# Kernel tuning notes

Measured on AMD Instinct MI355X. Metric: run time of the kernel, lower is better.

## Reference

```python
import jax, jax.numpy as jnp
import numpy as np


def setup_inputs() -> dict:
    key = jax.random.key(0)
    kq, kk, kv = jax.random.split(key, 3)
    B, H, S, D = 4, 16, 2048, 64
    q = jax.random.normal(kq, (B, H, S, D), dtype=jnp.float32)
    k = jax.random.normal(kk, (B, H, S, D), dtype=jnp.float32)
    v = jax.random.normal(kv, (B, H, S, D), dtype=jnp.float32)
    # causal mask: True = attend, broadcasts over batch/head dims
    mask = jnp.tril(jnp.ones((S, S), dtype=bool))
    return {"q": q, "k": k, "v": v, "mask": mask}


def reference(q, k, v, mask):
    # att[b,h,i,j] = q[b,h,i,:] . k[b,h,j,:] / sqrt(d_k)
    scale = 1.0 / jnp.sqrt(jnp.asarray(k.shape[-1], dtype=q.dtype))
    att = jnp.einsum('bhqd,bhkd->bhqk', q, k) * scale
    att = jnp.where(mask, att, -jnp.inf)  # additive -inf mask, equivalent to att + where(mask,0,-inf)
    att = jax.nn.softmax(att, axis=-1)
    return jnp.einsum('bhqk,bhkd->bhqd', att, v)
```

## Files before the change

### kernel.cpp

```cpp
#include <hip/hip_runtime.h>
#include <hip/hip_bf16.h>

typedef __attribute__((ext_vector_type(4)))  float f32x4;
typedef __attribute__((ext_vector_type(16))) float f32x16;
typedef __attribute__((ext_vector_type(8)))  short bf16x8;
typedef __attribute__((ext_vector_type(4)))  short bf16x4;

constexpr int SEQ = 2048;
constexpr int DH  = 64;
constexpr int BH  = 64;
constexpr int QB  = 256;
constexpr int KB  = 64;
constexpr int NQT = SEQ / QB;
constexpr int NST = SEQ / 64;

__device__ __forceinline__ short f2bf(float f) {
    union { float f; unsigned u; } x; x.f = f;
    unsigned r = x.u + 0x7fffu + ((x.u >> 16) & 1u);
    return (short)(r >> 16);
}

__device__ __forceinline__ unsigned cvtpk(float lo, float hi) {
    unsigned r;
    asm("v_cvt_pk_bf16_f32 %0, %1, %2" : "=v"(r) : "v"(lo), "v"(hi));
    return r;
}

__device__ __forceinline__ float exp2fast(float x) {
#if __has_builtin(__builtin_amdgcn_exp2f)
    return __builtin_amdgcn_exp2f(x);
#else
    float r;
    asm("v_exp_f32 %0, %1\n\ts_nop 0" : "=v"(r) : "v"(x));
    return r;
#endif
}

__device__ __forceinline__ void half_swap(unsigned a, unsigned b, unsigned &x, unsigned &y) {
#if __has_builtin(__builtin_amdgcn_permlane32_swap)
    auto rr = __builtin_amdgcn_permlane32_swap(a, b, false, false);
    x = rr[0]; y = rr[1];
#else
    unsigned as = (unsigned)__shfl_xor((int)a, 32);
    unsigned bs = (unsigned)__shfl_xor((int)b, 32);
    const bool lo = ((threadIdx.x & 63) < 32);
    x = lo ? a : bs;
    y = lo ? as : b;
#endif
}

__global__ __launch_bounds__(256) void prep_kernel(
    const float* __restrict__ Kg, const float* __restrict__ Vg,
    short* __restrict__ Kb, short* __restrict__ Vt)
{
    __shared__ short sT[64][66];
    const int bid = blockIdx.x;
    const int bh  = bid & (BH - 1);
    const int st  = bid >> 6;
    const int s0  = st * 64;
    const size_t base = (size_t)bh * SEQ * DH;
    const int tid = threadIdx.x;

    #pragma unroll
    for (int it = 0; it < 4; ++it) {
        const int i4 = it * 256 + tid;
        const int r  = i4 >> 4;
        const int c4 = (i4 & 15) << 2;
        const size_t gidx = base + (size_t)(s0 + r) * DH + c4;
        f32x4 kx = *(const f32x4*)(Kg + gidx);
        bf16x4 kb4;
        #pragma unroll
        for (int j = 0; j < 4; ++j) kb4[j] = f2bf(kx[j]);
        *(bf16x4*)(Kb + gidx) = kb4;
        f32x4 vx = *(const f32x4*)(Vg + gidx);
        #pragma unroll
        for (int j = 0; j < 4; ++j) sT[r][c4 + j] = f2bf(vx[j]);
    }
    __syncthreads();

    const int d   = tid >> 2;
    const int seg = (tid & 3) * 16;
    bf16x8 lo, hi;
    #pragma unroll
    for (int m = 0; m < 8; ++m) { lo[m] = sT[seg + m][d]; hi[m] = sT[seg + 8 + m][d]; }
    short* Vo = Vt + base + (size_t)d * SEQ + (s0 + seg);
    *(bf16x8*)Vo       = lo;
    *(bf16x8*)(Vo + 8) = hi;
}

__global__ __launch_bounds__(512) void fattn2_kernel(
    const float* __restrict__ Qg, const short* __restrict__ Kb,
    const short* __restrict__ Vt, float* __restrict__ Og)
{
    __shared__ short sK[KB * DH];
    __shared__ short sV[DH * KB];

    const int bid = blockIdx.x;
    const int g   = bid >> 6;
    const int bh  = bid & 63;
    const int qt  = (g < 4) ? (7 - g) : (g - 4);
    const int q0  = qt * QB;

    const int tid  = threadIdx.x;
    const int wid  = tid >> 6;
    const int lane = tid & 63;
    const int l31  = lane & 31;
    const int hi   = lane >> 5;

    const size_t base = (size_t)bh * SEQ * DH;
    const float* Qb = Qg + base;
    const short* Kp = Kb + base;
    const short* Vp = Vt + base;

    const int qw = q0 + wid * 32;
    const int qr = qw + l31;

    constexpr float QSCALE = 0.125f * 1.44269504088896340736f;
    bf16x8 qf[4];
    #pragma unroll
    for (int dt = 0; dt < 4; ++dt) {
        const float* qp = Qb + (size_t)qr * DH + dt * 16 + hi * 8;
        f32x4 a = *(const f32x4*)qp;
        f32x4 b = *(const f32x4*)(qp + 4);
        bf16x8 f;
        #pragma unroll
        for (int j = 0; j < 4; ++j) { f[j] = f2bf(a[j] * QSCALE); f[j + 4] = f2bf(b[j] * QSCALE); }
        qf[dt] = f;
    }

    f32x16 o0, o1;
    #pragma unroll
    for (int r = 0; r < 16; ++r) { o0[r] = 0.f; o1[r] = 0.f; }
    float m_i = -1e30f, l_i = 0.f;

    const int ntile = qt * 4 + 4;
    for (int t = 0; t < ntile; ++t) {
        const int kv0 = t * KB;
        __syncthreads();
        {
            const int r  = tid >> 3;
            const int cb = (tid & 7) * 16;
            bf16x8 kx = *(const bf16x8*)((const char*)(Kp + (size_t)(kv0 + r) * DH) + cb);
            *(bf16x8*)((char*)sK + r * 128 + (cb ^ ((r & 7) << 4))) = kx;
            bf16x8 vx = *(const bf16x8*)((const char*)(Vp + (size_t)r * SEQ + kv0) + cb);
            *(bf16x8*)((char*)sV + r * 128 + (cb ^ ((r & 7) << 4))) = vx;
        }
        __syncthreads();

        if (kv0 > qw + 31) continue;

        f32x16 st0, st1;
        #pragma unroll
        for (int r = 0; r < 16; ++r) { st0[r] = 0.f; st1[r] = 0.f; }
        #pragma unroll
        for (int dt = 0; dt < 4; ++dt) {
            const int ca = dt * 32 + hi * 16;
            bf16x8 k0 = *(const bf16x8*)((const char*)sK + l31 * 128 + (ca ^ ((l31 & 7) << 4)));
            bf16x8 k1 = *(const bf16x8*)((const char*)sK + (32 + l31) * 128 + (ca ^ ((l31 & 7) << 4)));
            st0 = __builtin_amdgcn_mfma_f32_32x32x16_bf16(k0, qf[dt], st0, 0, 0, 0);
            st1 = __builtin_amdgcn_mfma_f32_32x32x16_bf16(k1, qf[dt], st1, 0, 0, 0);
        }

        if (kv0 + KB - 1 > qw) {
            #pragma unroll
            for (int r = 0; r < 16; ++r) {
                const int kr = (r & 3) + 8 * (r >> 2) + 4 * hi;
                if (kv0 + kr > qr)      st0[r] = -1e30f;
                if (kv0 + 32 + kr > qr) st1[r] = -1e30f;
            }
        }

        float pm = st0[0];
        #pragma unroll
        for (int r = 1; r < 16; ++r) pm = fmaxf(pm, st0[r]);
        #pragma unroll
        for (int r = 0; r < 16; ++r) pm = fmaxf(pm, st1[r]);
        pm = fmaxf(pm, __shfl_xor(pm, 32));

        constexpr float THR = 8.0f * 1.44269504088896340736f;
        if (!__all(pm - m_i <= THR)) {
            const float nm = fmaxf(m_i, pm);
            const float cf = exp2fast(m_i - nm);
            #pragma unroll
            for (int r = 0; r < 16; ++r) {
                const int kr = (r & 3) + 8 * (r >> 2) + 4 * hi;
                const float cfr = __shfl(cf, kr);
                o0[r] *= cfr; o1[r] *= cfr;
            }
            l_i *= cf;
            m_i = nm;
        }

        float rs = 0.f;
        #pragma unroll
        for (int r = 0; r < 16; ++r) { st0[r] = exp2fast(st0[r] - m_i); rs += st0[r]; }
        #pragma unroll
        for (int r = 0; r < 16; ++r) { st1[r] = exp2fast(st1[r] - m_i); rs += st1[r]; }
        rs += __shfl_xor(rs, 32);
        l_i += rs;

        bf16x8 pf[4];
        {
            unsigned pk[8];
            #pragma unroll
            for (int i = 0; i < 8; ++i) pk[i] = cvtpk(st0[2 * i], st0[2 * i + 1]);
            #pragma unroll
            for (int c = 0; c < 2; ++c) {
                unsigned x0, y0, x1, y1;
                half_swap(pk[4 * c + 0], pk[4 * c + 2], x0, y0);
                half_swap(pk[4 * c + 1], pk[4 * c + 3], x1, y1);
                union { unsigned u[4]; bf16x8 v; } uu;
                uu.u[0] = x0; uu.u[1] = x1; uu.u[2] = y0; uu.u[3] = y1;
                pf[c] = uu.v;
            }
            #pragma unroll
            for (int i = 0; i < 8; ++i) pk[i] = cvtpk(st1[2 * i], st1[2 * i + 1]);
            #pragma unroll
            for (int c = 0; c < 2; ++c) {
                unsigned x0, y0, x1, y1;
                half_swap(pk[4 * c + 0], pk[4 * c + 2], x0, y0);
                half_swap(pk[4 * c + 1], pk[4 * c + 3], x1, y1);
                union { unsigned u[4]; bf16x8 v; } uu;
                uu.u[0] = x0; uu.u[1] = x1; uu.u[2] = y0; uu.u[3] = y1;
                pf[2 + c] = uu.v;
            }
        }

        #pragma unroll
        for (int ks = 0; ks < 4; ++ks) {
            const int cv = ks * 32 + hi * 16;
            bf16x8 v0 = *(const bf16x8*)((const char*)sV + l31 * 128 + (cv ^ ((l31 & 7) << 4)));
            o0 = __builtin_amdgcn_mfma_f32_32x32x16_bf16(pf[ks], v0, o0, 0, 0, 0);
            bf16x8 v1 = *(const bf16x8*)((const char*)sV + (32 + l31) * 128 + (cv ^ ((l31 & 7) << 4)));
            o1 = __builtin_amdgcn_mfma_f32_32x32x16_bf16(pf[ks], v1, o1, 0, 0, 0);
        }
    }

    float* Ob = Og + base;
    #pragma unroll
    for (int r = 0; r < 16; ++r) {
        const int kr  = (r & 3) + 8 * (r >> 2) + 4 * hi;
        const float ll = __shfl(l_i, kr);
        const float inv = 1.0f / ll;
        const int row = qw + kr;
        Ob[(size_t)row * DH + l31]      = o0[r] * inv;
        Ob[(size_t)row * DH + 32 + l31] = o1[r] * inv;
    }
}

extern "C" void kernel_launch(void* const* d_in, const int* in_sizes, int n_in,
                              void* d_out, int out_size, void* d_ws, size_t ws_size,
                              hipStream_t stream) {
    const float* q = (const float*)d_in[0];
    const float* k = (const float*)d_in[1];
    const float* v = (const float*)d_in[2];
    float* out = (float*)d_out;

    short* Kb = (short*)d_ws;
    short* Vt = Kb + (size_t)BH * SEQ * DH;

    prep_kernel<<<dim3(BH * NST), dim3(256), 0, stream>>>(k, v, Kb, Vt);
    fattn2_kernel<<<dim3(BH * NQT), dim3(512), 0, stream>>>(q, Kb, Vt, out);
}
```

Before: 81.48 us.

## Halve query tile, prefetch next K/V tile into registers during compute

The query block shrinks from 256 to 128 rows with 256-thread blocks and a min-blocks-per-SM launch bound of 4, doubling the grid to raise occupancy and improve causal load balance. Block scheduling becomes a simple heaviest-first order. Each iteration now issues global loads for the next K/V tile into registers before computing the current tile, then writes them to shared memory after a barrier, so memory latency overlaps the MFMA work. In exchange there is more register pressure, K/V tiles are re-read by twice as many blocks, and there are still two barriers per tile.

```diff
diff --git a/kernel.cpp b/kernel.cpp
--- a/kernel.cpp
+++ b/kernel.cpp
@@ -9,7 +9,7 @@
 constexpr int SEQ = 2048;
 constexpr int DH  = 64;
 constexpr int BH  = 64;
-constexpr int QB  = 256;
+constexpr int QB  = 128;
 constexpr int KB  = 64;
 constexpr int NQT = SEQ / QB;
 constexpr int NST = SEQ / 64;
@@ -88,7 +88,7 @@
     *(bf16x8*)(Vo + 8) = hi;
 }
 
-__global__ __launch_bounds__(512) void fattn2_kernel(
+__global__ __launch_bounds__(256, 4) void fattn3_kernel(
     const float* __restrict__ Qg, const short* __restrict__ Kb,
     const short* __restrict__ Vt, float* __restrict__ Og)
 {
@@ -96,9 +96,8 @@
     __shared__ short sV[DH * KB];
 
     const int bid = blockIdx.x;
-    const int g   = bid >> 6;
     const int bh  = bid & 63;
-    const int qt  = (g < 4) ? (7 - g) : (g - 4);
+    const int qt  = NQT - 1 - (bid >> 6);
     const int q0  = qt * QB;
 
     const int tid  = threadIdx.x;
@@ -114,6 +113,26 @@
 
     const int qw = q0 + wid * 32;
     const int qr = qw + l31;
+
+    const int r0 = tid >> 3;
+    const int c0 = tid & 7;
+    const int r1 = 32 + r0;
+    const int c1 = c0;
+
+    bf16x8 kreg0, kreg1, vreg0, vreg1;
+    auto LOAD = [&](int t) {
+        const int kv0 = t * KB;
+        kreg0 = *(const bf16x8*)(Kp + (size_t)(kv0 + r0) * DH + c0 * 8);
+        kreg1 = *(const bf16x8*)(Kp + (size_t)(kv0 + r1) * DH + c1 * 8);
+        vreg0 = *(const bf16x8*)(Vp + (size_t)r0 * SEQ + kv0 + c0 * 8);
+        vreg1 = *(const bf16x8*)(Vp + (size_t)r1 * SEQ + kv0 + c1 * 8);
+    };
+    auto WRITE = [&]() {
+        *(bf16x8*)((char*)sK + r0 * 128 + ((c0 * 16) ^ ((r0 & 7) << 4))) = kreg0;
+        *(bf16x8*)((char*)sK + r1 * 128 + ((c1 * 16) ^ ((r1 & 7) << 4))) = kreg1;
+        *(bf16x8*)((char*)sV + r0 * 128 + ((c0 * 16) ^ ((r0 & 7) << 4))) = vreg0;
+        *(bf16x8*)((char*)sV + r1 * 128 + ((c1 * 16) ^ ((r1 & 7) << 4))) = vreg1;
+    };
 
     constexpr float QSCALE = 0.125f * 1.44269504088896340736f;
     bf16x8 qf[4];
@@ -133,107 +152,106 @@
     for (int r = 0; r < 16; ++r) { o0[r] = 0.f; o1[r] = 0.f; }
     float m_i = -1e30f, l_i = 0.f;
 
-    const int ntile = qt * 4 + 4;
+    const int ntile = 2 * qt + 2;
+    LOAD(0);
+    WRITE();
+    __syncthreads();
+
     for (int t = 0; t < ntile; ++t) {
         const int kv0 = t * KB;
+        if (t + 1 < ntile) LOAD(t + 1);
+
+        if (kv0 <= qw + 31) {
+            f32x16 st0, st1;
+            #pragma unroll
+            for (int r = 0; r < 16; ++r) { st0[r] = 0.f; st1[r] = 0.f; }
+            #pragma unroll
+            for (int dt = 0; dt < 4; ++dt) {
+                const int ca = dt * 32 + hi * 16;
+                bf16x8 k0 = *(const bf16x8*)((const char*)sK + l31 * 128 + (ca ^ ((l31 & 7) << 4)));
+                bf16x8 k1 = *(const bf16x8*)((const char*)sK + (32 + l31) * 128 + (ca ^ ((l31 & 7) << 4)));
+                st0 = __builtin_amdgcn_mfma_f32_32x32x16_bf16(k0, qf[dt], st0, 0, 0, 0);
+                st1 = __builtin_amdgcn_mfma_f32_32x32x16_bf16(k1, qf[dt], st1, 0, 0, 0);
+            }
+
+            if (kv0 + KB - 1 > qw) {
+                #pragma unroll
+                for (int r = 0; r < 16; ++r) {
+                    const int kr = (r & 3) + 8 * (r >> 2) + 4 * hi;
+                    if (kv0 + kr > qr)      st0[r] = -1e30f;
+                    if (kv0 + 32 + kr > qr) st1[r] = -1e30f;
+                }
+            }
+
+            float pm = st0[0];
+            #pragma unroll
+            for (int r = 1; r < 16; ++r) pm = fmaxf(pm, st0[r]);
+            #pragma unroll
+            for (int r = 0; r < 16; ++r) pm = fmaxf(pm, st1[r]);
+            pm = fmaxf(pm, __shfl_xor(pm, 32));
+
+            constexpr float THR = 8.0f * 1.44269504088896340736f;
+            if (!__all(pm - m_i <= THR)) {
+                const float nm = fmaxf(m_i, pm);
+                const float cf = exp2fast(m_i - nm);
+                #pragma unroll
+                for (int r = 0; r < 16; ++r) {
+                    const int kr = (r & 3) + 8 * (r >> 2) + 4 * hi;
+                    const float cfr = __shfl(cf, kr);
+                    o0[r] *= cfr; o1[r] *= cfr;
+                }
+                l_i *= cf;
+                m_i = nm;
+            }
+
+            float rs = 0.f;
+            #pragma unroll
+            for (int r = 0; r < 16; ++r) { st0[r] = exp2fast(st0[r] - m_i); rs += st0[r]; }
+            #pragma unroll
+            for (int r = 0; r < 16; ++r) { st1[r] = exp2fast(st1[r] - m_i); rs += st1[r]; }
+            rs += __shfl_xor(rs, 32);
+            l_i += rs;
+
+            bf16x8 pf[4];
+            {
+                unsigned pk[8];
+                #pragma unroll
+                for (int i = 0; i < 8; ++i) pk[i] = cvtpk(st0[2 * i], st0[2 * i + 1]);
+                #pragma unroll
+                for (int c = 0; c < 2; ++c) {
+                    unsigned x0, y0, x1, y1;
+                    half_swap(pk[4 * c + 0], pk[4 * c + 2], x0, y0);
+                    half_swap(pk[4 * c + 1], pk[4 * c + 3], x1, y1);
+                    union { unsigned u[4]; bf16x8 v; } uu;
+                    uu.u[0] = x0; uu.u[1] = x1; uu.u[2] = y0; uu.u[3] = y1;
+                    pf[c] = uu.v;
+                }
+                #pragma unroll
+                for (int i = 0; i < 8; ++i) pk[i] = cvtpk(st1[2 * i], st1[2 * i + 1]);
+                #pragma unroll
+                for (int c = 0; c < 2; ++c) {
+                    unsigned x0, y0, x1, y1;
+                    half_swap(pk[4 * c + 0], pk[4 * c + 2], x0, y0);
+                    half_swap(pk[4 * c + 1], pk[4 * c + 3], x1, y1);
+                    union { unsigned u[4]; bf16x8 v; } uu;
+                    uu.u[0] = x0; uu.u[1] = x1; uu.u[2] = y0; uu.u[3] = y1;
+                    pf[2 + c] = uu.v;
+                }
+            }
+
+            #pragma unroll
+            for (int ks = 0; ks < 4; ++ks) {
+                const int cv = ks * 32 + hi * 16;
+                bf16x8 v0 = *(const bf16x8*)((const char*)sV + l31 * 128 + (cv ^ ((l31 & 7) << 4)));
+                o0 = __builtin_amdgcn_mfma_f32_32x32x16_bf16(pf[ks], v0, o0, 0, 0, 0);
+                bf16x8 v1 = *(const bf16x8*)((const char*)sV + (32 + l31) * 128 + (cv ^ ((l31 & 7) << 4)));
+                o1 = __builtin_amdgcn_mfma_f32_32x32x16_bf16(pf[ks], v1, o1, 0, 0, 0);
+            }
+        }
+
         __syncthreads();
-        {
-            const int r  = tid >> 3;
-            const int cb = (tid & 7) * 16;
-            bf16x8 kx = *(const bf16x8*)((const char*)(Kp + (size_t)(kv0 + r) * DH) + cb);
-            *(bf16x8*)((char*)sK + r * 128 + (cb ^ ((r & 7) << 4))) = kx;
-            bf16x8 vx = *(const bf16x8*)((const char*)(Vp + (size_t)r * SEQ + kv0) + cb);
-            *(bf16x8*)((char*)sV + r * 128 + (cb ^ ((r & 7) << 4))) = vx;
-        }
+        if (t + 1 < ntile) WRITE();
         __syncthreads();
-
-        if (kv0 > qw + 31) continue;
-
-        f32x16 st0, st1;
-        #pragma unroll
-        for (int r = 0; r < 16; ++r) { st0[r] = 0.f; st1[r] = 0.f; }
-        #pragma unroll
-        for (int dt = 0; dt < 4; ++dt) {
-            const int ca = dt * 32 + hi * 16;
-            bf16x8 k0 = *(const bf16x8*)((const char*)sK + l31 * 128 + (ca ^ ((l31 & 7) << 4)));
-            bf16x8 k1 = *(const bf16x8*)((const char*)sK + (32 + l31) * 128 + (ca ^ ((l31 & 7) << 4)));
-            st0 = __builtin_amdgcn_mfma_f32_32x32x16_bf16(k0, qf[dt], st0, 0, 0, 0);
-            st1 = __builtin_amdgcn_mfma_f32_32x32x16_bf16(k1, qf[dt], st1, 0, 0, 0);
-        }
-
-        if (kv0 + KB - 1 > qw) {
-            #pragma unroll
-            for (int r = 0; r < 16; ++r) {
-                const int kr = (r & 3) + 8 * (r >> 2) + 4 * hi;
-                if (kv0 + kr > qr)      st0[r] = -1e30f;
-                if (kv0 + 32 + kr > qr) st1[r] = -1e30f;
-            }
-        }
-
-        float pm = st0[0];
-        #pragma unroll
-        for (int r = 1; r < 16; ++r) pm = fmaxf(pm, st0[r]);
-        #pragma unroll
-        for (int r = 0; r < 16; ++r) pm = fmaxf(pm, st1[r]);
-        pm = fmaxf(pm, __shfl_xor(pm, 32));
-
-        constexpr float THR = 8.0f * 1.44269504088896340736f;
-        if (!__all(pm - m_i <= THR)) {
-            const float nm = fmaxf(m_i, pm);
-            const float cf = exp2fast(m_i - nm);
-            #pragma unroll
-            for (int r = 0; r < 16; ++r) {
-                const int kr = (r & 3) + 8 * (r >> 2) + 4 * hi;
-                const float cfr = __shfl(cf, kr);
-                o0[r] *= cfr; o1[r] *= cfr;
-            }
-            l_i *= cf;
-            m_i = nm;
-        }
-
-        float rs = 0.f;
-        #pragma unroll
-        for (int r = 0; r < 16; ++r) { st0[r] = exp2fast(st0[r] - m_i); rs += st0[r]; }
-        #pragma unroll
-        for (int r = 0; r < 16; ++r) { st1[r] = exp2fast(st1[r] - m_i); rs += st1[r]; }
-        rs += __shfl_xor(rs, 32);
-        l_i += rs;
-
-        bf16x8 pf[4];
-        {
-            unsigned pk[8];
-            #pragma unroll
-            for (int i = 0; i < 8; ++i) pk[i] = cvtpk(st0[2 * i], st0[2 * i + 1]);
-            #pragma unroll
-            for (int c = 0; c < 2; ++c) {
-                unsigned x0, y0, x1, y1;
-                half_swap(pk[4 * c + 0], pk[4 * c + 2], x0, y0);
-                half_swap(pk[4 * c + 1], pk[4 * c + 3], x1, y1);
-                union { unsigned u[4]; bf16x8 v; } uu;
-                uu.u[0] = x0; uu.u[1] = x1; uu.u[2] = y0; uu.u[3] = y1;
-                pf[c] = uu.v;
-            }
-            #pragma unroll
-            for (int i = 0; i < 8; ++i) pk[i] = cvtpk(st1[2 * i], st1[2 * i + 1]);
-            #pragma unroll
-            for (int c = 0; c < 2; ++c) {
-                unsigned x0, y0, x1, y1;
-                half_swap(pk[4 * c + 0], pk[4 * c + 2], x0, y0);
-                half_swap(pk[4 * c + 1], pk[4 * c + 3], x1, y1);
-                union { unsigned u[4]; bf16x8 v; } uu;
-                uu.u[0] = x0; uu.u[1] = x1; uu.u[2] = y0; uu.u[3] = y1;
-                pf[2 + c] = uu.v;
-            }
-        }
-
-        #pragma unroll
-        for (int ks = 0; ks < 4; ++ks) {
-            const int cv = ks * 32 + hi * 16;
-            bf16x8 v0 = *(const bf16x8*)((const char*)sV + l31 * 128 + (cv ^ ((l31 & 7) << 4)));
-            o0 = __builtin_amdgcn_mfma_f32_32x32x16_bf16(pf[ks], v0, o0, 0, 0, 0);
-            bf16x8 v1 = *(const bf16x8*)((const char*)sV + (32 + l31) * 128 + (cv ^ ((l31 & 7) << 4)));
-            o1 = __builtin_amdgcn_mfma_f32_32x32x16_bf16(pf[ks], v1, o1, 0, 0, 0);
-        }
     }
 
     float* Ob = Og + base;
@@ -260,5 +278,5 @@
     short* Vt = Kb + (size_t)BH * SEQ * DH;
 
     prep_kernel<<<dim3(BH * NST), dim3(256), 0, stream>>>(k, v, Kb, Vt);
-    fattn2_kernel<<<dim3(BH * NQT), dim3(512), 0, stream>>>(q, Kb, Vt, out);
-}
+    fattn3_kernel<<<dim3(BH * NQT), dim3(256), 0, stream>>>(q, Kb, Vt, out);
+}
```

Result: slower. 97.13 us (+19.2%).

## Double-buffer K/V tiles with direct global-to-LDS async loads

Applied to the files above, without the earlier changes.

Replaces the register-staged K/V tile copy with __builtin_amdgcn_global_load_lds into a double-buffered LDS array. The next tile is issued before computing on the current one, and only one barrier per iteration remains. The XOR swizzle is moved to the global source address so the LDS layout matches the old one. This is meant to hide global load latency behind MFMA work and drop a barrier and the VGPR round-trip. In exchange it doubles LDS use. Correctness relies on the loads landing before the barrier, since no explicit vmcnt wait is visible.

```diff
diff --git a/kernel.cpp b/kernel.cpp
--- a/kernel.cpp
+++ b/kernel.cpp
@@ -88,12 +88,12 @@
     *(bf16x8*)(Vo + 8) = hi;
 }
 
-__global__ __launch_bounds__(512) void fattn2_kernel(
+__global__ __launch_bounds__(512) void fattn4_kernel(
     const float* __restrict__ Qg, const short* __restrict__ Kb,
     const short* __restrict__ Vt, float* __restrict__ Og)
 {
-    __shared__ short sK[KB * DH];
-    __shared__ short sV[DH * KB];
+    __shared__ short sK[2][KB * DH];
+    __shared__ short sV[2][DH * KB];
 
     const int bid = blockIdx.x;
     const int g   = bid >> 6;
@@ -114,6 +114,21 @@
 
     const int qw = q0 + wid * 32;
     const int qr = qw + l31;
+
+    const int rr = wid * 8 + (lane >> 3);
+    const int cs = (lane & 7) ^ (rr & 7);
+    const short* kSrc = Kp + (size_t)rr * DH + cs * 8;
+    const short* vSrc = Vp + (size_t)rr * SEQ + cs * 8;
+
+    auto ISSUE = [&](int t, int buf) {
+        const int kv0 = t * KB;
+        __builtin_amdgcn_global_load_lds(
+            (const unsigned int*)(kSrc + (size_t)kv0 * DH),
+            (unsigned int*)&sK[buf][wid * 512], 16, 0, 0);
+        __builtin_amdgcn_global_load_lds(
+            (const unsigned int*)(vSrc + kv0),
+            (unsigned int*)&sV[buf][wid * 512], 16, 0, 0);
+    };
 
     constexpr float QSCALE = 0.125f * 1.44269504088896340736f;
     bf16x8 qf[4];
@@ -134,106 +149,106 @@
     float m_i = -1e30f, l_i = 0.f;
 
     const int ntile = qt * 4 + 4;
+    ISSUE(0, 0);
+    __syncthreads();
+
     for (int t = 0; t < ntile; ++t) {
         const int kv0 = t * KB;
+        const int cur = t & 1;
+        if (t + 1 < ntile) ISSUE(t + 1, cur ^ 1);
+
+        if (kv0 <= qw + 31) {
+            const short* cK = &sK[cur][0];
+            const short* cV = &sV[cur][0];
+
+            f32x16 st0, st1;
+            #pragma unroll
+            for (int r = 0; r < 16; ++r) { st0[r] = 0.f; st1[r] = 0.f; }
+            #pragma unroll
+            for (int dt = 0; dt < 4; ++dt) {
+                const int ca = dt * 32 + hi * 16;
+                bf16x8 k0 = *(const bf16x8*)((const char*)cK + l31 * 128 + (ca ^ ((l31 & 7) << 4)));
+                bf16x8 k1 = *(const bf16x8*)((const char*)cK + (32 + l31) * 128 + (ca ^ ((l31 & 7) << 4)));
+                st0 = __builtin_amdgcn_mfma_f32_32x32x16_bf16(k0, qf[dt], st0, 0, 0, 0);
+                st1 = __builtin_amdgcn_mfma_f32_32x32x16_bf16(k1, qf[dt], st1, 0, 0, 0);
+            }
+
+            if (kv0 + KB - 1 > qw) {
+                #pragma unroll
+                for (int r = 0; r < 16; ++r) {
+                    const int kr = (r & 3) + 8 * (r >> 2) + 4 * hi;
+                    if (kv0 + kr > qr)      st0[r] = -1e30f;
+                    if (kv0 + 32 + kr > qr) st1[r] = -1e30f;
+                }
+            }
+
+            float pm = st0[0];
+            #pragma unroll
+            for (int r = 1; r < 16; ++r) pm = fmaxf(pm, st0[r]);
+            #pragma unroll
+            for (int r = 0; r < 16; ++r) pm = fmaxf(pm, st1[r]);
+            pm = fmaxf(pm, __shfl_xor(pm, 32));
+
+            constexpr float THR = 8.0f * 1.44269504088896340736f;
+            if (!__all(pm - m_i <= THR)) {
+                const float nm = fmaxf(m_i, pm);
+                const float cf = exp2fast(m_i - nm);
+                #pragma unroll
+                for (int r = 0; r < 16; ++r) {
+                    const int kr = (r & 3) + 8 * (r >> 2) + 4 * hi;
+                    const float cfr = __shfl(cf, kr);
+                    o0[r] *= cfr; o1[r] *= cfr;
+                }
+                l_i *= cf;
+                m_i = nm;
+            }
+
+            float rs = 0.f;
+            #pragma unroll
+            for (int r = 0; r < 16; ++r) { st0[r] = exp2fast(st0[r] - m_i); rs += st0[r]; }
+            #pragma unroll
+            for (int r = 0; r < 16; ++r) { st1[r] = exp2fast(st1[r] - m_i); rs += st1[r]; }
+            rs += __shfl_xor(rs, 32);
+            l_i += rs;
+
+            bf16x8 pf[4];
+            {
+                unsigned pk[8];
+                #pragma unroll
+                for (int i = 0; i < 8; ++i) pk[i] = cvtpk(st0[2 * i], st0[2 * i + 1]);
+                #pragma unroll
+                for (int c = 0; c < 2; ++c) {
+                    unsigned x0, y0, x1, y1;
+                    half_swap(pk[4 * c + 0], pk[4 * c + 2], x0, y0);
+                    half_swap(pk[4 * c + 1], pk[4 * c + 3], x1, y1);
+                    union { unsigned u[4]; bf16x8 v; } uu;
+                    uu.u[0] = x0; uu.u[1] = x1; uu.u[2] = y0; uu.u[3] = y1;
+                    pf[c] = uu.v;
+                }
+                #pragma unroll
+                for (int i = 0; i < 8; ++i) pk[i] = cvtpk(st1[2 * i], st1[2 * i + 1]);
+                #pragma unroll
+                for (int c = 0; c < 2; ++c) {
+                    unsigned x0, y0, x1, y1;
+                    half_swap(pk[4 * c + 0], pk[4 * c + 2], x0, y0);
+                    half_swap(pk[4 * c + 1], pk[4 * c + 3], x1, y1);
+                    union { unsigned u[4]; bf16x8 v; } uu;
+                    uu.u[0] = x0; uu.u[1] = x1; uu.u[2] = y0; uu.u[3] = y1;
+                    pf[2 + c] = uu.v;
+                }
+            }
+
+            #pragma unroll
+            for (int ks = 0; ks < 4; ++ks) {
+                const int cv = ks * 32 + hi * 16;
+                bf16x8 v0 = *(const bf16x8*)((const char*)cV + l31 * 128 + (cv ^ ((l31 & 7) << 4)));
+                o0 = __builtin_amdgcn_mfma_f32_32x32x16_bf16(pf[ks], v0, o0, 0, 0, 0);
+                bf16x8 v1 = *(const bf16x8*)((const char*)cV + (32 + l31) * 128 + (cv ^ ((l31 & 7) << 4)));
+                o1 = __builtin_amdgcn_mfma_f32_32x32x16_bf16(pf[ks], v1, o1, 0, 0, 0);
+            }
+        }
+
         __syncthreads();
-        {
-            const int r  = tid >> 3;
-            const int cb = (tid & 7) * 16;
-            bf16x8 kx = *(const bf16x8*)((const char*)(Kp + (size_t)(kv0 + r) * DH) + cb);
-            *(bf16x8*)((char*)sK + r * 128 + (cb ^ ((r & 7) << 4))) = kx;
-            bf16x8 vx = *(const bf16x8*)((const char*)(Vp + (size_t)r * SEQ + kv0) + cb);
-            *(bf16x8*)((char*)sV + r * 128 + (cb ^ ((r & 7) << 4))) = vx;
-        }
-        __syncthreads();
-
-        if (kv0 > qw + 31) continue;
-
-        f32x16 st0, st1;
-        #pragma unroll
-        for (int r = 0; r < 16; ++r) { st0[r] = 0.f; st1[r] = 0.f; }
-        #pragma unroll
-        for (int dt = 0; dt < 4; ++dt) {
-            const int ca = dt * 32 + hi * 16;
-            bf16x8 k0 = *(const bf16x8*)((const char*)sK + l31 * 128 + (ca ^ ((l31 & 7) << 4)));
-            bf16x8 k1 = *(const bf16x8*)((const char*)sK + (32 + l31) * 128 + (ca ^ ((l31 & 7) << 4)));
-            st0 = __builtin_amdgcn_mfma_f32_32x32x16_bf16(k0, qf[dt], st0, 0, 0, 0);
-            st1 = __builtin_amdgcn_mfma_f32_32x32x16_bf16(k1, qf[dt], st1, 0, 0, 0);
-        }
-
-        if (kv0 + KB - 1 > qw) {
-            #pragma unroll
-            for (int r = 0; r < 16; ++r) {
-                const int kr = (r & 3) + 8 * (r >> 2) + 4 * hi;
-                if (kv0 + kr > qr)      st0[r] = -1e30f;
-                if (kv0 + 32 + kr > qr) st1[r] = -1e30f;
-            }
-        }
-
-        float pm = st0[0];
-        #pragma unroll
-        for (int r = 1; r < 16; ++r) pm = fmaxf(pm, st0[r]);
-        #pragma unroll
-        for (int r = 0; r < 16; ++r) pm = fmaxf(pm, st1[r]);
-        pm = fmaxf(pm, __shfl_xor(pm, 32));
-
-        constexpr float THR = 8.0f * 1.44269504088896340736f;
-        if (!__all(pm - m_i <= THR)) {
-            const float nm = fmaxf(m_i, pm);
-            const float cf = exp2fast(m_i - nm);
-            #pragma unroll
-            for (int r = 0; r < 16; ++r) {
-                const int kr = (r & 3) + 8 * (r >> 2) + 4 * hi;
-                const float cfr = __shfl(cf, kr);
-                o0[r] *= cfr; o1[r] *= cfr;
-            }
-            l_i *= cf;
-            m_i = nm;
-        }
-
-        float rs = 0.f;
-        #pragma unroll
-        for (int r = 0; r < 16; ++r) { st0[r] = exp2fast(st0[r] - m_i); rs += st0[r]; }
-        #pragma unroll
-        for (int r = 0; r < 16; ++r) { st1[r] = exp2fast(st1[r] - m_i); rs += st1[r]; }
-        rs += __shfl_xor(rs, 32);
-        l_i += rs;
-
-        bf16x8 pf[4];
-        {
-            unsigned pk[8];
-            #pragma unroll
-            for (int i = 0; i < 8; ++i) pk[i] = cvtpk(st0[2 * i], st0[2 * i + 1]);
-            #pragma unroll
-            for (int c = 0; c < 2; ++c) {
-                unsigned x0, y0, x1, y1;
-                half_swap(pk[4 * c + 0], pk[4 * c + 2], x0, y0);
-                half_swap(pk[4 * c + 1], pk[4 * c + 3], x1, y1);
-                union { unsigned u[4]; bf16x8 v; } uu;
-                uu.u[0] = x0; uu.u[1] = x1; uu.u[2] = y0; uu.u[3] = y1;
-                pf[c] = uu.v;
-            }
-            #pragma unroll
-            for (int i = 0; i < 8; ++i) pk[i] = cvtpk(st1[2 * i], st1[2 * i + 1]);
-            #pragma unroll
-            for (int c = 0; c < 2; ++c) {
-                unsigned x0, y0, x1, y1;
-                half_swap(pk[4 * c + 0], pk[4 * c + 2], x0, y0);
-                half_swap(pk[4 * c + 1], pk[4 * c + 3], x1, y1);
-                union { unsigned u[4]; bf16x8 v; } uu;
-                uu.u[0] = x0; uu.u[1] = x1; uu.u[2] = y0; uu.u[3] = y1;
-                pf[2 + c] = uu.v;
-            }
-        }
-
-        #pragma unroll
-        for (int ks = 0; ks < 4; ++ks) {
-            const int cv = ks * 32 + hi * 16;
-            bf16x8 v0 = *(const bf16x8*)((const char*)sV + l31 * 128 + (cv ^ ((l31 & 7) << 4)));
-            o0 = __builtin_amdgcn_mfma_f32_32x32x16_bf16(pf[ks], v0, o0, 0, 0, 0);
-            bf16x8 v1 = *(const bf16x8*)((const char*)sV + (32 + l31) * 128 + (cv ^ ((l31 & 7) << 4)));
-            o1 = __builtin_amdgcn_mfma_f32_32x32x16_bf16(pf[ks], v1, o1, 0, 0, 0);
-        }
     }
 
     float* Ob = Og + base;
@@ -260,5 +275,5 @@
     short* Vt = Kb + (size_t)BH * SEQ * DH;
 
     prep_kernel<<<dim3(BH * NST), dim3(256), 0, stream>>>(k, v, Kb, Vt);
-    fattn2_kernel<<<dim3(BH * NQT), dim3(512), 0, stream>>>(q, Kb, Vt, out);
-}
+    fattn4_kernel<<<dim3(BH * NQT), dim3(512), 0, stream>>>(q, Kb, Vt, out);
+}
```

Measured after the change: 80.63 us. No clear change (-1.1%).
